# Optimization experiments

Hardware: AMD Instinct MI355X
Metric: run time of the kernel (lower is better)

## Reference

```python
import jax, jax.numpy as jnp
import numpy as np

DIM = 3072
H = 24
HD = DIM // H  # 128
B = 1
IMG = 2048
TXT = 256


def _apply_rope(x, cos, sin):
    # x: [B, H, S, D]; cos/sin: [S, D]. Diffusers-style interleaved rotate-half:
    # pairs (x0, x1) -> (x0*c - x1*s, x1*c + x0*s)
    x1 = x[..., 0::2]
    x2 = x[..., 1::2]
    x_rot = jnp.stack([-x2, x1], axis=-1).reshape(x.shape)
    return x * cos + x_rot * sin


def setup_inputs() -> dict:
    key = jax.random.key(0)
    ks = jax.random.split(key, 26)

    def w(k):
        return jax.random.normal(k, (DIM, DIM), jnp.float32) * 0.02

    def b(k):
        return jax.random.normal(k, (DIM,), jnp.float32) * 0.02

    return {
        "image_hidden_states": jax.random.normal(ks[0], (B, IMG, DIM), jnp.float32),
        "text_hidden_states": jax.random.normal(ks[1], (B, TXT, DIM), jnp.float32),
        "img_cos": jax.random.uniform(ks[2], (IMG, HD), jnp.float32),
        "img_sin": jax.random.uniform(ks[3], (IMG, HD), jnp.float32),
        "txt_cos": jax.random.uniform(ks[4], (TXT, HD), jnp.float32),
        "txt_sin": jax.random.uniform(ks[5], (TXT, HD), jnp.float32),
        "Wq": w(ks[6]), "bq": b(ks[7]),
        "Wk": w(ks[8]), "bk": b(ks[9]),
        "Wv": w(ks[10]), "bv": b(ks[11]),
        "Waq": w(ks[12]), "baq": b(ks[13]),
        "Wak": w(ks[14]), "bak": b(ks[15]),
        "Wav": w(ks[16]), "bav": b(ks[17]),
        "Wo": w(ks[18]), "bo": b(ks[19]),
        "Wao": w(ks[20]), "bao": b(ks[21]),
    }


def reference(image_hidden_states, text_hidden_states, img_cos, img_sin,
              txt_cos, txt_sin, Wq, bq, Wk, bk, Wv, bv, Waq, baq, Wak, bak,
              Wav, bav, Wo, bo, Wao, bao):
    Bz, Si, D = image_hidden_states.shape
    St = text_hidden_states.shape[1]

    def proj(x, W, b):  # torch nn.Linear: x @ W.T + b
        return x @ W.T + b

    def heads(x, S):  # [B,S,D] -> [B,H,S,HD]
        return x.reshape(Bz, S, H, HD).transpose(0, 2, 1, 3)

    q_img = heads(proj(image_hidden_states, Wq, bq), Si)
    k_img = heads(proj(image_hidden_states, Wk, bk), Si)
    v_img = heads(proj(image_hidden_states, Wv, bv), Si)
    q_txt = heads(proj(text_hidden_states, Waq, baq), St)
    k_txt = heads(proj(text_hidden_states, Wak, bak), St)
    v_txt = heads(proj(text_hidden_states, Wav, bav), St)

    q_img = _apply_rope(q_img, img_cos, img_sin)
    k_img = _apply_rope(k_img, img_cos, img_sin)
    q_txt = _apply_rope(q_txt, txt_cos, txt_sin)
    k_txt = _apply_rope(k_txt, txt_cos, txt_sin)

    # joint sequence: text first, then image
    q = jnp.concatenate([q_txt, q_img], axis=2)
    k = jnp.concatenate([k_txt, k_img], axis=2)
    v = jnp.concatenate([v_txt, v_img], axis=2)

    scale = HD ** -0.5
    scores = jnp.einsum('bhqd,bhkd->bhqk', q, k) * scale  # [B,H,S,S]
    attn = jax.nn.softmax(scores, axis=-1)
    out = jnp.einsum('bhqk,bhkd->bhqd', attn, v)
    out = out.transpose(0, 2, 1, 3).reshape(Bz, St + Si, D)

    txt_out = out[:, :St] @ Wao.T + bao
    img_out = out[:, St:] @ Wo.T + bo
    return (img_out, txt_out)
```

## Files before the change

kernel.cpp:

```cpp
#include <hip/hip_runtime.h>
#include <cstdint>
#include <cstddef>

typedef __bf16 bf16x8 __attribute__((ext_vector_type(8)));
typedef __bf16 bf16x4 __attribute__((ext_vector_type(4)));
typedef float  f32x4  __attribute__((ext_vector_type(4)));

#define S_TXT 256
#define S_IMG 2048
#define S_TOT 2304
#define NHEAD 24
#define HDIM  128
#define DMODEL 3072

static constexpr size_t SZ_QKV  = (size_t)NHEAD * S_TOT * HDIM;
static constexpr size_t SZ_AO   = (size_t)S_TOT * DMODEL;
static constexpr size_t SZ_XIMG = (size_t)S_IMG * DMODEL;
static constexpr size_t SZ_XTXT = (size_t)S_TXT * DMODEL;
static constexpr size_t SZ_W    = (size_t)DMODEL * DMODEL;

#define QSCALE (0.08838834764831845f * 1.4426950408889634f)

__device__ __forceinline__ f32x4 mfma16(bf16x8 a, bf16x8 b, f32x4 c) {
  return __builtin_amdgcn_mfma_f32_16x16x32_bf16(a, b, c, 0, 0, 0);
}

__device__ __forceinline__ float fexp2(float x) {
  return __builtin_amdgcn_exp2f(x);
}

__global__ __launch_bounds__(256) void cvt_f32_bf16(const float* __restrict__ in,
                                                    __bf16* __restrict__ out, int n) {
  int i = (blockIdx.x * 256 + threadIdx.x) * 8;
  if (i + 8 > n) return;
  f32x4 a = *(const f32x4*)(in + i);
  f32x4 b = *(const f32x4*)(in + i + 4);
  bf16x8 r;
  r[0]=(__bf16)a[0]; r[1]=(__bf16)a[1]; r[2]=(__bf16)a[2]; r[3]=(__bf16)a[3];
  r[4]=(__bf16)b[0]; r[5]=(__bf16)b[1]; r[6]=(__bf16)b[2]; r[7]=(__bf16)b[3];
  *(bf16x8*)(out + i) = r;
}

struct CWArgs { const float* s[6]; __bf16* d[6]; };
__global__ __launch_bounds__(256) void cvt_w(CWArgs a) {
  const float* in = a.s[blockIdx.y];
  __bf16* out = a.d[blockIdx.y];
  size_t i = ((size_t)blockIdx.x * 256 + threadIdx.x) * 8;
  f32x4 x = *(const f32x4*)(in + i);
  f32x4 y = *(const f32x4*)(in + i + 4);
  bf16x8 r;
  r[0]=(__bf16)x[0]; r[1]=(__bf16)x[1]; r[2]=(__bf16)x[2]; r[3]=(__bf16)x[3];
  r[4]=(__bf16)y[0]; r[5]=(__bf16)y[1]; r[6]=(__bf16)y[2]; r[7]=(__bf16)y[3];
  *(bf16x8*)(out + i) = r;
}

__global__ __launch_bounds__(256) void rope_kernel(__bf16* __restrict__ Qb, __bf16* __restrict__ Kb,
    const float* __restrict__ icos, const float* __restrict__ isin,
    const float* __restrict__ tcos, const float* __restrict__ tsin) {
  size_t idx = ((size_t)blockIdx.x * 256 + threadIdx.x) * 8;
  __bf16* X; float mult;
  if (blockIdx.y) { X = Kb; mult = 1.0f; }
  else            { X = Qb; mult = QSCALE; }
  int d = (int)(idx & 127);
  int s = (int)((idx >> 7) % S_TOT);
  const float *cp, *sp; int ss;
  if (s < S_TXT) { cp = tcos; sp = tsin; ss = s; }
  else           { cp = icos; sp = isin; ss = s - S_TXT; }
  const float* cb = cp + (size_t)ss * HDIM + d;
  const float* sb = sp + (size_t)ss * HDIM + d;
  f32x4 c0 = *(const f32x4*)(cb);
  f32x4 c1 = *(const f32x4*)(cb + 4);
  f32x4 s0 = *(const f32x4*)(sb);
  f32x4 s1 = *(const f32x4*)(sb + 4);
  bf16x8 x = *(const bf16x8*)(X + idx);
  float xf[8];
  #pragma unroll
  for (int j = 0; j < 8; ++j) xf[j] = (float)x[j];
  bf16x8 o;
  o[0] = (__bf16)((xf[0]*c0[0] - xf[1]*s0[0]) * mult);
  o[1] = (__bf16)((xf[1]*c0[1] + xf[0]*s0[1]) * mult);
  o[2] = (__bf16)((xf[2]*c0[2] - xf[3]*s0[2]) * mult);
  o[3] = (__bf16)((xf[3]*c0[3] + xf[2]*s0[3]) * mult);
  o[4] = (__bf16)((xf[4]*c1[0] - xf[5]*s1[0]) * mult);
  o[5] = (__bf16)((xf[5]*c1[1] + xf[4]*s1[1]) * mult);
  o[6] = (__bf16)((xf[6]*c1[2] - xf[7]*s1[2]) * mult);
  o[7] = (__bf16)((xf[7]*c1[3] + xf[6]*s1[3]) * mult);
  *(bf16x8*)(X + idx) = o;
}

__global__ __launch_bounds__(128) void transpose_v(const __bf16* __restrict__ V,
                                                   __bf16* __restrict__ Vt) {
  int h = blockIdx.y, s0 = blockIdx.x * 64, d = threadIdx.x;
  const __bf16* src = V + ((size_t)h * S_TOT + s0) * HDIM + d;
  __bf16 tmp[64];
  #pragma unroll
  for (int k = 0; k < 64; ++k) tmp[k] = src[(size_t)k * HDIM];
  __bf16* dst = Vt + ((size_t)h * HDIM + d) * S_TOT + s0;
  #pragma unroll
  for (int k = 0; k < 8; ++k) {
    bf16x8 v;
    #pragma unroll
    for (int j = 0; j < 8; ++j) v[j] = tmp[k*8 + j];
    *(bf16x8*)(dst + k*8) = v;
  }
}

struct GBArgs {
  const __bf16* A;
  const __bf16* W0[3];
  const __bf16* W1[3];
  const float* b0[3]; const float* b1[3];
  void* O0[3]; void* O1[3];
};

template<int MODE>
__global__ __launch_bounds__(256) void gemm_bf(GBArgs ga) {
  const int tid = threadIdx.x;
  const int lane = tid & 63, wave = tid >> 6;
  const int wr = wave >> 1, wc = wave & 1;
  const int g = lane >> 4, lr = lane & 15;
  const int x7 = lr & 7;

  const int hw = (int)blockIdx.x;
  const int xcd = hw & 7, idx = hw >> 3;
  const int bx = idx % 18;
  const int nglob = (MODE == 0) ? (xcd * 9 + idx / 18) : (xcd * 3 + idx / 18);
  const int wsel = (MODE == 0) ? nglob / 24 : 0;
  const int ny   = (MODE == 0) ? nglob % 24 : nglob;
  const int m0 = bx * 128;
  const int n0 = ny * 128;
  const bool txt = (MODE == 0) ? (m0 >= S_IMG) : (m0 < S_TXT);
  const __bf16* Wf  = txt ? ga.W1[wsel] : ga.W0[wsel];
  const float* bias = txt ? ga.b1[wsel] : ga.b0[wsel];

  __shared__ __align__(16) __bf16 As[128 * 64];
  __shared__ __align__(16) __bf16 Bs[128 * 64];

  const int sr8 = lane >> 3;
  const int sch = (lane & 7) ^ sr8;
  const __bf16* Ap = ga.A + (size_t)(m0 + wave * 8 + sr8) * DMODEL + sch * 8;
  const __bf16* Bp = Wf   + (size_t)(n0 + wave * 8 + sr8) * DMODEL + sch * 8;

  f32x4 acc[4][4];
  #pragma unroll
  for (int i = 0; i < 4; ++i)
    #pragma unroll
    for (int j = 0; j < 4; ++j) acc[i][j] = (f32x4){0.f,0.f,0.f,0.f};

#define GLD(dst, srcp) { \
    _Pragma("unroll") \
    for (int i_ = 0; i_ < 4; ++i_) \
      __builtin_amdgcn_global_load_lds( \
          (const __attribute__((address_space(1))) void*)((srcp) + (size_t)i_ * 32 * DMODEL), \
          (__attribute__((address_space(3))) void*)((char*)(dst) + i_ * 4096 + wave * 1024), \
          16, 0, 0); }

  for (int kt = 0; kt < DMODEL / 64; ++kt) {
    GLD(As, Ap + kt * 64);
    GLD(Bs, Bp + kt * 64);
    __syncthreads();
    #pragma unroll
    for (int ks = 0; ks < 2; ++ks) {
      bf16x8 af[4], bf[4];
      #pragma unroll
      for (int i = 0; i < 4; ++i)
        af[i] = *(const bf16x8*)((char*)As + (wr*64 + i*16 + lr) * 128 + (((ks*4 + g) ^ x7) << 4));
      #pragma unroll
      for (int j = 0; j < 4; ++j)
        bf[j] = *(const bf16x8*)((char*)Bs + (wc*64 + j*16 + lr) * 128 + (((ks*4 + g) ^ x7) << 4));
      __builtin_amdgcn_s_setprio(1);
      #pragma unroll
      for (int i = 0; i < 4; ++i)
        #pragma unroll
        for (int j = 0; j < 4; ++j)
          acc[i][j] = mfma16(af[i], bf[j], acc[i][j]);
      __builtin_amdgcn_s_setprio(0);
    }
    __syncthreads();
  }
#undef GLD

  float bv[4];
  #pragma unroll
  for (int j = 0; j < 4; ++j) bv[j] = bias[n0 + wc*64 + j*16 + lr];

  if (MODE == 0) {
    const int head = ny;
    const int sbase = txt ? (m0 - S_IMG) : (m0 + S_TXT);
    if (wsel == 2) {
      __bf16* Vt = (__bf16*)ga.O0[2];
      #pragma unroll
      for (int i = 0; i < 4; ++i) {
        const int s0 = sbase + wr*64 + i*16 + g*4;
        #pragma unroll
        for (int j = 0; j < 4; ++j) {
          const int hd = wc*64 + j*16 + lr;
          bf16x4 pk;
          #pragma unroll
          for (int r = 0; r < 4; ++r) pk[r] = (__bf16)(acc[i][j][r] + bv[j]);
          *(bf16x4*)(Vt + ((size_t)(head * HDIM + hd)) * S_TOT + s0) = pk;
        }
      }
    } else {
      __bf16* Qp = (__bf16*)ga.O0[wsel];
      #pragma unroll
      for (int i = 0; i < 4; ++i)
        #pragma unroll
        for (int j = 0; j < 4; ++j)
          #pragma unroll
          for (int r = 0; r < 4; ++r) {
            int s  = sbase + wr*64 + i*16 + g*4 + r;
            int hd = wc*64 + j*16 + lr;
            Qp[((size_t)head * S_TOT + s) * HDIM + hd] = (__bf16)(acc[i][j][r] + bv[j]);
          }
    }
  } else {
    float* Cf = (float*)(txt ? ga.O1[0] : ga.O0[0]);
    const int rbase = txt ? m0 : (m0 - S_TXT);
    #pragma unroll
    for (int i = 0; i < 4; ++i)
      #pragma unroll
      for (int j = 0; j < 4; ++j)
        #pragma unroll
        for (int r = 0; r < 4; ++r) {
          int m = rbase + wr*64 + i*16 + g*4 + r;
          int n = n0 + wc*64 + j*16 + lr;
          Cf[(size_t)m * DMODEL + n] = acc[i][j][r] + bv[j];
        }
  }
}

struct GArgs {
  const __bf16* A;
  const float* W0[3]; const float* W1[3];
  const float* b0[3]; const float* b1[3];
  void* O0[3]; void* O1[3];
};

#define NT 48

template<int MODE>
__global__ __launch_bounds__(256, 1) void gemm_all(GArgs ga) {
  const int tid = threadIdx.x;
  const int lane = tid & 63, wave = tid >> 6;
  const int wr = wave >> 1, wc = wave & 1;
  const int g = lane >> 4, lr = lane & 15;
  const int x7 = lr & 7;

  const int hw = (int)blockIdx.x;
  const int xcd = hw & 7, idx = hw >> 3;
  const int bx = idx % 18;
  const int nglob = (MODE == 0) ? (xcd * 9 + idx / 18) : (xcd * 3 + idx / 18);
  const int wsel = (MODE == 0) ? nglob / 24 : 0;
  const int ny   = (MODE == 0) ? nglob % 24 : nglob;
  const int m0 = bx * 128;
  const int n0 = ny * 128;
  const bool txt = (MODE == 0) ? (m0 >= S_IMG) : (m0 < S_TXT);
  const float* Wf   = txt ? ga.W1[wsel] : ga.W0[wsel];
  const float* bias = txt ? ga.b1[wsel] : ga.b0[wsel];

  __shared__ __align__(16) __bf16 As[2][128 * 64];
  __shared__ __align__(16) __bf16 Bs[128 * 64];

  const int sr8 = lane >> 3;
  const int sch = (lane & 7) ^ sr8;
  const __bf16* Ap = ga.A + (size_t)(m0 + wave * 8 + sr8) * DMODEL + sch * 8;

  const int wrow = tid >> 3;
  const int wch  = tid & 7;
  const float* Bp = Wf + (size_t)(n0 + wrow) * DMODEL + wch * 8;
  const int bwoff = wrow * 128 + ((wch ^ (wrow & 7)) << 4);

  f32x4 acc[4][4];
  #pragma unroll
  for (int i = 0; i < 4; ++i)
    #pragma unroll
    for (int j = 0; j < 4; ++j) acc[i][j] = (f32x4){0.f,0.f,0.f,0.f};

  f32x4 pre[4][2];

#define VSEP asm volatile("" ::: "memory")
#define ISSUE_A(kt, buf) { \
    const __bf16* Apk = Ap + (kt) * 64; \
    char* dst = (char*)(&As[(buf)][0]) + wave * 1024; \
    _Pragma("unroll") \
    for (int i_ = 0; i_ < 4; ++i_) \
      __builtin_amdgcn_global_load_lds( \
          (const __attribute__((address_space(1))) void*)(Apk + (size_t)i_ * 32 * DMODEL), \
          (__attribute__((address_space(3))) void*)(dst + i_ * 4096), 16, 0, 0); }
#define ISSUE_B(kt) { \
    const float* Bpk = Bp + (kt) * 64; \
    _Pragma("unroll") \
    for (int p_ = 0; p_ < 4; ++p_) { \
      pre[p_][0] = *(const f32x4*)(Bpk + (size_t)p_ * 32 * DMODEL); \
      pre[p_][1] = *(const f32x4*)(Bpk + (size_t)p_ * 32 * DMODEL + 4); } }
#define WRITE_B() { \
    _Pragma("unroll") \
    for (int p_ = 0; p_ < 4; ++p_) { \
      bf16x8 bw_; \
      _Pragma("unroll") \
      for (int j_ = 0; j_ < 4; ++j_) { \
        bw_[j_]     = (__bf16)pre[p_][0][j_]; \
        bw_[4 + j_] = (__bf16)pre[p_][1][j_]; } \
      *(bf16x8*)((char*)Bs + p_ * 4096 + bwoff) = bw_; } }
#define COMPUTE(buf) { \
    _Pragma("unroll") \
    for (int ks_ = 0; ks_ < 2; ++ks_) { \
      bf16x8 af_[4], bf_[4]; \
      _Pragma("unroll") \
      for (int i_ = 0; i_ < 4; ++i_) \
        af_[i_] = *(const bf16x8*)((char*)(&As[(buf)][0]) + (wr*64 + i_*16 + lr) * 128 + (((ks_*4 + g) ^ x7) << 4)); \
      _Pragma("unroll") \
      for (int j_ = 0; j_ < 4; ++j_) \
        bf_[j_] = *(const bf16x8*)((char*)Bs + (wc*64 + j_*16 + lr) * 128 + (((ks_*4 + g) ^ x7) << 4)); \
      __builtin_amdgcn_s_setprio(1); \
      _Pragma("unroll") \
      for (int i_ = 0; i_ < 4; ++i_) \
        _Pragma("unroll") \
        for (int j_ = 0; j_ < 4; ++j_) \
          acc[i_][j_] = mfma16(af_[i_], bf_[j_], acc[i_][j_]); \
      __builtin_amdgcn_s_setprio(0); } }

  ISSUE_B(0);        VSEP;
  ISSUE_A(0, 0);     VSEP;
  asm volatile("s_waitcnt vmcnt(4)" ::: "memory");
  WRITE_B();
  asm volatile("s_waitcnt vmcnt(0) lgkmcnt(0)" ::: "memory");
  __builtin_amdgcn_s_barrier();
  VSEP;

  for (int t = 0; t < NT - 2; t += 2) {
    ISSUE_A(t + 1, 1);  VSEP;
    ISSUE_B(t + 1);     VSEP;
    COMPUTE(0);
    __builtin_amdgcn_s_barrier();
    asm volatile("s_waitcnt vmcnt(0)" ::: "memory");
    WRITE_B();
    asm volatile("s_waitcnt lgkmcnt(0)" ::: "memory");
    __builtin_amdgcn_s_barrier();
    VSEP;
    ISSUE_A(t + 2, 0);  VSEP;
    ISSUE_B(t + 2);     VSEP;
    COMPUTE(1);
    __builtin_amdgcn_s_barrier();
    asm volatile("s_waitcnt vmcnt(0)" ::: "memory");
    WRITE_B();
    asm volatile("s_waitcnt lgkmcnt(0)" ::: "memory");
    __builtin_amdgcn_s_barrier();
    VSEP;
  }

  ISSUE_A(NT - 1, 1);  VSEP;
  ISSUE_B(NT - 1);     VSEP;
  COMPUTE(0);
  __builtin_amdgcn_s_barrier();
  asm volatile("s_waitcnt vmcnt(0)" ::: "memory");
  WRITE_B();
  asm volatile("s_waitcnt lgkmcnt(0)" ::: "memory");
  __builtin_amdgcn_s_barrier();
  COMPUTE(1);

#undef VSEP
#undef ISSUE_A
#undef ISSUE_B
#undef WRITE_B
#undef COMPUTE

  float bv[4];
  #pragma unroll
  for (int j = 0; j < 4; ++j) bv[j] = bias[n0 + wc*64 + j*16 + lr];

  if (MODE == 0) {
    __bf16* Qp = (__bf16*)(txt ? ga.O1[wsel] : ga.O0[wsel]);
    const int sbase = txt ? (m0 - S_IMG) : (m0 + S_TXT);
    #pragma unroll
    for (int i = 0; i < 4; ++i)
      #pragma unroll
      for (int j = 0; j < 4; ++j)
        #pragma unroll
        for (int r = 0; r < 4; ++r) {
          int s  = sbase + wr*64 + i*16 + g*4 + r;
          int hd = wc*64 + j*16 + lr;
          Qp[((size_t)ny * S_TOT + s) * HDIM + hd] = (__bf16)(acc[i][j][r] + bv[j]);
        }
  } else {
    float* Cf = (float*)(txt ? ga.O1[0] : ga.O0[0]);
    const int rbase = txt ? m0 : (m0 - S_TXT);
    #pragma unroll
    for (int i = 0; i < 4; ++i)
      #pragma unroll
      for (int j = 0; j < 4; ++j)
        #pragma unroll
        for (int r = 0; r < 4; ++r) {
          int m = rbase + wr*64 + i*16 + g*4 + r;
          int n = n0 + wc*64 + j*16 + lr;
          Cf[(size_t)m * DMODEL + n] = acc[i][j][r] + bv[j];
        }
  }
}

__global__ __launch_bounds__(256, 2) void flash_attn(
    const __bf16* __restrict__ Qg, const __bf16* __restrict__ Kg,
    const __bf16* __restrict__ Vt, __bf16* __restrict__ Og)
{
  const int h = blockIdx.y;
  const int q0 = blockIdx.x * 64;
  const int tid = threadIdx.x;
  const int lane = tid & 63, wave = tid >> 6;
  const int g = lane >> 4, lr = lane & 15;
  const int x7 = lr & 7;

  __shared__ __align__(16) __bf16 Kl[64 * 128];
  __shared__ __align__(16) __bf16 Vl[128 * 64];
  __shared__ __align__(16) __bf16 Pl[4][16 * 64];
  char* Kc = (char*)Kl;
  char* Vc = (char*)Vl;
  char* Pc = (char*)&Pl[wave][0];

  bf16x8 ones;
  #pragma unroll
  for (int j = 0; j < 8; ++j) ones[j] = (__bf16)1.0f;

  bf16x8 qf[4];
  {
    const __bf16* qp = Qg + ((size_t)h * S_TOT + q0 + wave*16 + lr) * HDIM + g * 8;
    #pragma unroll
    for (int kb = 0; kb < 4; ++kb) qf[kb] = *(const bf16x8*)(qp + kb * 32);
  }

  f32x4 acc[8];
  #pragma unroll
  for (int i = 0; i < 8; ++i) acc[i] = (f32x4){0.f,0.f,0.f,0.f};
  float lrow[4] = {0.f, 0.f, 0.f, 0.f};

  const int krow = tid >> 4, kc = tid & 15;
  const int vrow = tid >> 3, vc = tid & 7;
  const __bf16* Kbase = Kg + (size_t)h * S_TOT * HDIM;
  const __bf16* Vbase = Vt + (size_t)h * HDIM * S_TOT;

  const int kwoff = krow * 256 + ((kc ^ (krow & 7)) << 4);
  const int vwoff = vrow * 128 + ((vc ^ (vrow & 7)) << 4);

  bf16x8 kreg[4], vreg[4];
  #pragma unroll
  for (int i = 0; i < 4; ++i) {
    kreg[i] = *(const bf16x8*)(Kbase + (size_t)(i*16 + krow) * HDIM + kc * 8);
    vreg[i] = *(const bf16x8*)(Vbase + (size_t)(i*32 + vrow) * S_TOT + vc * 8);
  }

  for (int t = 0; t < S_TOT / 64; ++t) {
    asm volatile("" ::: "memory");
    __builtin_amdgcn_s_barrier();
    asm volatile("" ::: "memory");
    #pragma unroll
    for (int i = 0; i < 4; ++i) {
      *(bf16x8*)(Kc + kwoff + i * 4096) = kreg[i];
      *(bf16x8*)(Vc + vwoff + i * 4096) = vreg[i];
    }
    if (t + 1 < S_TOT / 64) {
      int kv1 = (t + 1) * 64;
      #pragma unroll
      for (int i = 0; i < 4; ++i) {
        kreg[i] = *(const bf16x8*)(Kbase + (size_t)(kv1 + i*16 + krow) * HDIM + kc * 8);
        vreg[i] = *(const bf16x8*)(Vbase + (size_t)(i*32 + vrow) * S_TOT + kv1 + vc * 8);
      }
    }
    asm volatile("s_waitcnt lgkmcnt(0)" ::: "memory");
    __builtin_amdgcn_s_barrier();
    asm volatile("" ::: "memory");

    f32x4 sc[4];
    __builtin_amdgcn_s_setprio(1);
    #pragma unroll
    for (int kb = 0; kb < 4; ++kb) {
      f32x4 s4 = (f32x4){0.f,0.f,0.f,0.f};
      #pragma unroll
      for (int dk = 0; dk < 4; ++dk) {
        bf16x8 kf = *(const bf16x8*)(Kc + (kb*16 + lr) * 256 + (((dk*4 + g) ^ x7) << 4));
        s4 = mfma16(qf[dk], kf, s4);
      }
      sc[kb] = s4;
    }
    __builtin_amdgcn_s_setprio(0);

    #pragma unroll
    for (int kb = 0; kb < 4; ++kb)
      #pragma unroll
      for (int r = 0; r < 4; ++r)
        sc[kb][r] = fexp2(sc[kb][r]);

    #pragma unroll
    for (int kb = 0; kb < 4; ++kb)
      #pragma unroll
      for (int r = 0; r < 4; ++r) {
        int row = g*4 + r;
        *(__bf16*)(Pc + (((row * 128) + (kb*16 + lr) * 2) ^ ((row & 7) << 4))) = (__bf16)sc[kb][r];
      }

    bf16x8 ap0 = *(const bf16x8*)(Pc + ((lr * 128 + g * 16) ^ (x7 << 4)));
    bf16x8 ap1 = *(const bf16x8*)(Pc + ((lr * 128 + (4 + g) * 16) ^ (x7 << 4)));

    f32x4 ls = (f32x4){0.f, 0.f, 0.f, 0.f};
    ls = mfma16(ap0, ones, ls);
    ls = mfma16(ap1, ones, ls);
    #pragma unroll
    for (int r = 0; r < 4; ++r) lrow[r] += ls[r];

    __builtin_amdgcn_s_setprio(1);
    #pragma unroll
    for (int db = 0; db < 8; ++db) {
      bf16x8 v0 = *(const bf16x8*)(Vc + (db*16 + lr) * 128 + ((g ^ x7) << 4));
      bf16x8 v1 = *(const bf16x8*)(Vc + (db*16 + lr) * 128 + (((4 + g) ^ x7) << 4));
      acc[db] = mfma16(ap0, v0, acc[db]);
      acc[db] = mfma16(ap1, v1, acc[db]);
    }
    __builtin_amdgcn_s_setprio(0);
  }

  float rinv[4];
  #pragma unroll
  for (int r = 0; r < 4; ++r) rinv[r] = 1.f / lrow[r];
  #pragma unroll
  for (int db = 0; db < 8; ++db)
    #pragma unroll
    for (int r = 0; r < 4; ++r) {
      int s = q0 + wave*16 + g*4 + r;
      Og[(size_t)s * DMODEL + h * HDIM + db*16 + lr] = (__bf16)(acc[db][r] * rinv[r]);
    }
}

extern "C" void kernel_launch(void* const* d_in, const int* in_sizes, int n_in,
                              void* d_out, int out_size, void* d_ws, size_t ws_size,
                              hipStream_t stream) {
  const float* x_img   = (const float*)d_in[0];
  const float* x_txt   = (const float*)d_in[1];
  const float* img_cos = (const float*)d_in[2];
  const float* img_sin = (const float*)d_in[3];
  const float* txt_cos = (const float*)d_in[4];
  const float* txt_sin = (const float*)d_in[5];
  const float* Wq  = (const float*)d_in[6];  const float* bq  = (const float*)d_in[7];
  const float* Wk  = (const float*)d_in[8];  const float* bk  = (const float*)d_in[9];
  const float* Wv  = (const float*)d_in[10]; const float* bv  = (const float*)d_in[11];
  const float* Waq = (const float*)d_in[12]; const float* baq = (const float*)d_in[13];
  const float* Wak = (const float*)d_in[14]; const float* bak = (const float*)d_in[15];
  const float* Wav = (const float*)d_in[16]; const float* bav = (const float*)d_in[17];
  const float* Wo  = (const float*)d_in[18]; const float* bo  = (const float*)d_in[19];
  const float* Wao = (const float*)d_in[20]; const float* bao = (const float*)d_in[21];

  __bf16* ws = (__bf16*)d_ws;
  __bf16* Qb  = ws;
  __bf16* Kb  = Qb + SZ_QKV;
  __bf16* Vb  = Kb + SZ_QKV;
  __bf16* Vtb = Vb + SZ_QKV;
  __bf16* AO  = Vtb + SZ_QKV;
  __bf16* XI  = AO + SZ_AO;
  __bf16* XT  = XI + SZ_XIMG;
  __bf16* Wbf = XI + SZ_AO;

  const size_t need_big = (5 * SZ_QKV + SZ_AO + 6 * SZ_W) * sizeof(__bf16);
  const bool big = ws_size >= need_big;

  float* out_img = (float*)d_out;
  float* out_txt = out_img + (size_t)S_IMG * DMODEL;

  cvt_f32_bf16<<<dim3((unsigned)(SZ_XIMG/2048)), 256, 0, stream>>>(x_img, XI, (int)SZ_XIMG);
  cvt_f32_bf16<<<dim3((unsigned)(SZ_XTXT/2048)), 256, 0, stream>>>(x_txt, XT, (int)SZ_XTXT);

  if (big) {
    CWArgs cw{};
    const float* wsrc[6] = {Wq, Wk, Wv, Waq, Wak, Wav};
    for (int i = 0; i < 6; ++i) { cw.s[i] = wsrc[i]; cw.d[i] = Wbf + (size_t)i * SZ_W; }
    cvt_w<<<dim3((unsigned)(SZ_W/2048), 6), 256, 0, stream>>>(cw);

    GBArgs gb{};
    gb.A = XI;
    gb.W0[0] = Wbf;            gb.W0[1] = Wbf + SZ_W;     gb.W0[2] = Wbf + 2*SZ_W;
    gb.W1[0] = Wbf + 3*SZ_W;   gb.W1[1] = Wbf + 4*SZ_W;   gb.W1[2] = Wbf + 5*SZ_W;
    gb.b0[0] = bq;  gb.b0[1] = bk;  gb.b0[2] = bv;
    gb.b1[0] = baq; gb.b1[1] = bak; gb.b1[2] = bav;
    gb.O0[0] = Qb;  gb.O0[1] = Kb;  gb.O0[2] = Vtb;
    gb.O1[0] = Qb;  gb.O1[1] = Kb;  gb.O1[2] = Vtb;
    gemm_bf<0><<<dim3(1296), 256, 0, stream>>>(gb);
    rope_kernel<<<dim3(3456, 2), 256, 0, stream>>>(Qb, Kb, img_cos, img_sin, txt_cos, txt_sin);
  } else {
    GArgs gq{};
    gq.A = XI;
    gq.W0[0] = Wq;  gq.W0[1] = Wk;  gq.W0[2] = Wv;
    gq.W1[0] = Waq; gq.W1[1] = Wak; gq.W1[2] = Wav;
    gq.b0[0] = bq;  gq.b0[1] = bk;  gq.b0[2] = bv;
    gq.b1[0] = baq; gq.b1[1] = bak; gq.b1[2] = bav;
    gq.O0[0] = Qb;  gq.O0[1] = Kb;  gq.O0[2] = Vb;
    gq.O1[0] = Qb;  gq.O1[1] = Kb;  gq.O1[2] = Vb;
    gemm_all<0><<<dim3(1296), 256, 0, stream>>>(gq);
    rope_kernel<<<dim3(3456, 2), 256, 0, stream>>>(Qb, Kb, img_cos, img_sin, txt_cos, txt_sin);
    transpose_v<<<dim3(36, 24), 128, 0, stream>>>(Vb, Vtb);
  }

  flash_attn<<<dim3(36, 24), 256, 0, stream>>>(Qb, Kb, Vtb, AO);

  if (big) {
    CWArgs cw{};
    cw.s[0] = Wo;  cw.d[0] = Wbf;
    cw.s[1] = Wao; cw.d[1] = Wbf + SZ_W;
    cvt_w<<<dim3((unsigned)(SZ_W/2048), 2), 256, 0, stream>>>(cw);

    GBArgs go{};
    go.A = AO;
    go.W0[0] = Wbf;       go.W1[0] = Wbf + SZ_W;
    go.b0[0] = bo;  go.b1[0] = bao;
    go.O0[0] = out_img; go.O1[0] = out_txt;
    gemm_bf<1><<<dim3(432), 256, 0, stream>>>(go);
  } else {
    GArgs go{};
    go.A = AO;
    go.W0[0] = Wo;  go.W1[0] = Wao;
    go.b0[0] = bo;  go.b1[0] = bao;
    go.O0[0] = out_img; go.O1[0] = out_txt;
    gemm_all<1><<<dim3(432), 256, 0, stream>>>(go);
  }

  (void)in_sizes; (void)n_in; (void)out_size;
}
```

Baseline: 412.7 us.

## Double-buffer flash-attention K/V via direct global-to-LDS loads; batch all weight conversions

After: 438.4 us. 6.2% more time.

```diff
diff --git a/kernel.cpp b/kernel.cpp
--- a/kernel.cpp
+++ b/kernel.cpp
@@ -41,7 +41,7 @@
   *(bf16x8*)(out + i) = r;
 }
 
-struct CWArgs { const float* s[6]; __bf16* d[6]; };
+struct CWArgs { const float* s[8]; __bf16* d[8]; };
 __global__ __launch_bounds__(256) void cvt_w(CWArgs a) {
   const float* in = a.s[blockIdx.y];
   __bf16* out = a.d[blockIdx.y];
@@ -410,16 +410,19 @@
   const int g = lane >> 4, lr = lane & 15;
   const int x7 = lr & 7;
 
-  __shared__ __align__(16) __bf16 Kl[64 * 128];
-  __shared__ __align__(16) __bf16 Vl[128 * 64];
+  __shared__ __align__(16) __bf16 Kl[2][64 * 128];
+  __shared__ __align__(16) __bf16 Vl[2][128 * 64];
   __shared__ __align__(16) __bf16 Pl[4][16 * 64];
-  char* Kc = (char*)Kl;
-  char* Vc = (char*)Vl;
   char* Pc = (char*)&Pl[wave][0];
 
   bf16x8 ones;
   #pragma unroll
   for (int j = 0; j < 8; ++j) ones[j] = (__bf16)1.0f;
+
+  const int k_r = tid >> 4, k_c = (tid & 15) ^ ((tid >> 4) & 7);
+  const int v_r = tid >> 3, v_c = (tid & 7) ^ ((tid >> 3) & 7);
+  const __bf16* Kbase = Kg + (size_t)h * S_TOT * HDIM;
+  const __bf16* Vbase = Vt + (size_t)h * HDIM * S_TOT;
 
   bf16x8 qf[4];
   {
@@ -433,41 +436,30 @@
   for (int i = 0; i < 8; ++i) acc[i] = (f32x4){0.f,0.f,0.f,0.f};
   float lrow[4] = {0.f, 0.f, 0.f, 0.f};
 
-  const int krow = tid >> 4, kc = tid & 15;
-  const int vrow = tid >> 3, vc = tid & 7;
-  const __bf16* Kbase = Kg + (size_t)h * S_TOT * HDIM;
-  const __bf16* Vbase = Vt + (size_t)h * HDIM * S_TOT;
-
-  const int kwoff = krow * 256 + ((kc ^ (krow & 7)) << 4);
-  const int vwoff = vrow * 128 + ((vc ^ (vrow & 7)) << 4);
-
-  bf16x8 kreg[4], vreg[4];
-  #pragma unroll
-  for (int i = 0; i < 4; ++i) {
-    kreg[i] = *(const bf16x8*)(Kbase + (size_t)(i*16 + krow) * HDIM + kc * 8);
-    vreg[i] = *(const bf16x8*)(Vbase + (size_t)(i*32 + vrow) * S_TOT + vc * 8);
-  }
+#define VSEP asm volatile("" ::: "memory")
+#define ISSUE_KV(t, buf) { \
+    _Pragma("unroll") \
+    for (int i_ = 0; i_ < 4; ++i_) \
+      __builtin_amdgcn_global_load_lds( \
+          (const __attribute__((address_space(1))) void*)(Kbase + (size_t)((t)*64 + i_*16 + k_r) * HDIM + k_c * 8), \
+          (__attribute__((address_space(3))) void*)((char*)&Kl[(buf)][0] + i_ * 4096 + wave * 1024), 16, 0, 0); \
+    _Pragma("unroll") \
+    for (int i_ = 0; i_ < 4; ++i_) \
+      __builtin_amdgcn_global_load_lds( \
+          (const __attribute__((address_space(1))) void*)(Vbase + (size_t)(i_*32 + v_r) * S_TOT + (t)*64 + v_c * 8), \
+          (__attribute__((address_space(3))) void*)((char*)&Vl[(buf)][0] + i_ * 4096 + wave * 1024), 16, 0, 0); }
+
+  ISSUE_KV(0, 0);  VSEP;
+  asm volatile("s_waitcnt vmcnt(0)" ::: "memory");
+  __builtin_amdgcn_s_barrier();
+  VSEP;
 
   for (int t = 0; t < S_TOT / 64; ++t) {
-    asm volatile("" ::: "memory");
-    __builtin_amdgcn_s_barrier();
-    asm volatile("" ::: "memory");
-    #pragma unroll
-    for (int i = 0; i < 4; ++i) {
-      *(bf16x8*)(Kc + kwoff + i * 4096) = kreg[i];
-      *(bf16x8*)(Vc + vwoff + i * 4096) = vreg[i];
-    }
-    if (t + 1 < S_TOT / 64) {
-      int kv1 = (t + 1) * 64;
-      #pragma unroll
-      for (int i = 0; i < 4; ++i) {
-        kreg[i] = *(const bf16x8*)(Kbase + (size_t)(kv1 + i*16 + krow) * HDIM + kc * 8);
-        vreg[i] = *(const bf16x8*)(Vbase + (size_t)(i*32 + vrow) * S_TOT + kv1 + vc * 8);
-      }
-    }
-    asm volatile("s_waitcnt lgkmcnt(0)" ::: "memory");
-    __builtin_amdgcn_s_barrier();
-    asm volatile("" ::: "memory");
+    const int buf = t & 1;
+    const char* Kc = (const char*)&Kl[buf][0];
+    const char* Vc = (const char*)&Vl[buf][0];
+    if (t + 1 < S_TOT / 64) { ISSUE_KV(t + 1, buf ^ 1); }
+    VSEP;
 
     f32x4 sc[4];
     __builtin_amdgcn_s_setprio(1);
@@ -515,7 +507,15 @@
       acc[db] = mfma16(ap1, v1, acc[db]);
     }
     __builtin_amdgcn_s_setprio(0);
-  }
+
+    if (t + 1 < S_TOT / 64) {
+      asm volatile("s_waitcnt vmcnt(0)" ::: "memory");
+      __builtin_amdgcn_s_barrier();
+      VSEP;
+    }
+  }
+#undef ISSUE_KV
+#undef VSEP
 
   float rinv[4];
   #pragma unroll
@@ -557,8 +557,10 @@
   __bf16* XT  = XI + SZ_XIMG;
   __bf16* Wbf = XI + SZ_AO;
 
-  const size_t need_big = (5 * SZ_QKV + SZ_AO + 6 * SZ_W) * sizeof(__bf16);
-  const bool big = ws_size >= need_big;
+  const size_t need6 = (5 * SZ_QKV + SZ_AO + 6 * SZ_W) * sizeof(__bf16);
+  const size_t need8 = (5 * SZ_QKV + SZ_AO + 8 * SZ_W) * sizeof(__bf16);
+  const bool big8 = ws_size >= need8;
+  const bool big  = ws_size >= need6;
 
   float* out_img = (float*)d_out;
   float* out_txt = out_img + (size_t)S_IMG * DMODEL;
@@ -568,9 +570,10 @@
 
   if (big) {
     CWArgs cw{};
-    const float* wsrc[6] = {Wq, Wk, Wv, Waq, Wak, Wav};
-    for (int i = 0; i < 6; ++i) { cw.s[i] = wsrc[i]; cw.d[i] = Wbf + (size_t)i * SZ_W; }
-    cvt_w<<<dim3((unsigned)(SZ_W/2048), 6), 256, 0, stream>>>(cw);
+    const float* wsrc[8] = {Wq, Wk, Wv, Waq, Wak, Wav, Wo, Wao};
+    const int nw = big8 ? 8 : 6;
+    for (int i = 0; i < nw; ++i) { cw.s[i] = wsrc[i]; cw.d[i] = Wbf + (size_t)i * SZ_W; }
+    cvt_w<<<dim3((unsigned)(SZ_W/2048), (unsigned)nw), 256, 0, stream>>>(cw);
 
     GBArgs gb{};
     gb.A = XI;
@@ -599,14 +602,19 @@
   flash_attn<<<dim3(36, 24), 256, 0, stream>>>(Qb, Kb, Vtb, AO);
 
   if (big) {
-    CWArgs cw{};
-    cw.s[0] = Wo;  cw.d[0] = Wbf;
-    cw.s[1] = Wao; cw.d[1] = Wbf + SZ_W;
-    cvt_w<<<dim3((unsigned)(SZ_W/2048), 2), 256, 0, stream>>>(cw);
-
+    const __bf16 *WoB, *WaoB;
+    if (big8) {
+      WoB = Wbf + 6*SZ_W;  WaoB = Wbf + 7*SZ_W;
+    } else {
+      CWArgs cw{};
+      cw.s[0] = Wo;  cw.d[0] = Wbf;
+      cw.s[1] = Wao; cw.d[1] = Wbf + SZ_W;
+      cvt_w<<<dim3((unsigned)(SZ_W/2048), 2), 256, 0, stream>>>(cw);
+      WoB = Wbf;  WaoB = Wbf + SZ_W;
+    }
     GBArgs go{};
     go.A = AO;
-    go.W0[0] = Wbf;       go.W1[0] = Wbf + SZ_W;
+    go.W0[0] = WoB;       go.W1[0] = WaoB;
     go.b0[0] = bo;  go.b1[0] = bao;
     go.O0[0] = out_img; go.O1[0] = out_txt;
     gemm_bf<1><<<dim3(432), 256, 0, stream>>>(go);
```
